# Performance work log

Hardware: AMD Instinct MI355X
Metric: run time of the kernel (lower is better)

Reference implementation:

```python
import jax, jax.numpy as jnp
import numpy as np

B = 65536

def _conv(x, w, stride=(1, 1), padding='VALID', groups=1):
    return jax.lax.conv_general_dilated(
        x, w, window_strides=stride, padding=padding,
        dimension_numbers=('NCHW', 'OIHW', 'NCHW'), feature_group_count=groups)

def _lstm_step(x, h, c, w_ih, w_hh, b_ih, b_hh):
    # PyTorch gate order: i, f, g, o
    gates = x @ w_ih.T + h @ w_hh.T + b_ih + b_hh
    i, f, g, o = jnp.split(gates, 4, axis=-1)
    c_new = jax.nn.sigmoid(f) * c + jax.nn.sigmoid(i) * jnp.tanh(g)
    h_new = jax.nn.sigmoid(o) * jnp.tanh(c_new)
    return h_new, c_new


def setup_inputs() -> dict:
    key = jax.random.key(0)
    ks = jax.random.split(key, 32)
    s = 0.1
    inp = {
        'x': jax.random.normal(ks[0], (B, 3, 41), jnp.float32),
        'lstm1_h': jax.random.normal(ks[1], (B, 64), jnp.float32),
        'lstm1_b': jax.random.normal(ks[2], (B, 64), jnp.float32),
        'lstm2_h': jax.random.normal(ks[3], (B, 64), jnp.float32),
        'lstm2_b': jax.random.normal(ks[4], (B, 64), jnp.float32),
        # conv stack params
        'conv_dw_w': jax.random.normal(ks[5], (1, 1, 3, 3), jnp.float32) * s,
        'conv_pw_w': jax.random.normal(ks[6], (16, 1, 1, 1), jnp.float32) * s,
        'conv_pw_b': jax.random.normal(ks[7], (16,), jnp.float32) * s,
        'sep1_dw_w': jax.random.normal(ks[8], (16, 1, 1, 3), jnp.float32) * s,
        'sep1_pw_w': jax.random.normal(ks[9], (16, 16, 1, 1), jnp.float32) * s,
        'sep1_pw_b': jax.random.normal(ks[10], (16,), jnp.float32) * s,
        'sep2_dw_w': jax.random.normal(ks[11], (16, 1, 1, 3), jnp.float32) * s,
        'sep2_pw_w': jax.random.normal(ks[12], (16, 16, 1, 1), jnp.float32) * s,
        'sep2_pw_b': jax.random.normal(ks[13], (16,), jnp.float32) * s,
        # lstm1: input 80, hidden 64
        'w_ih1': jax.random.normal(ks[14], (256, 80), jnp.float32) * s,
        'w_hh1': jax.random.normal(ks[15], (256, 64), jnp.float32) * s,
        'b_ih1': jax.random.normal(ks[16], (256,), jnp.float32) * s,
        'b_hh1': jax.random.normal(ks[17], (256,), jnp.float32) * s,
        # lstm2: input 64, hidden 64
        'w_ih2': jax.random.normal(ks[18], (256, 64), jnp.float32) * s,
        'w_hh2': jax.random.normal(ks[19], (256, 64), jnp.float32) * s,
        'b_ih2': jax.random.normal(ks[20], (256,), jnp.float32) * s,
        'b_hh2': jax.random.normal(ks[21], (256,), jnp.float32) * s,
        # fc head
        'fc1_w': jax.random.normal(ks[22], (32, 128), jnp.float32) * s,
        'fc1_b': jax.random.normal(ks[23], (32,), jnp.float32) * s,
        'fc2_w': jax.random.normal(ks[24], (1, 32), jnp.float32) * s,
        'fc2_b': jax.random.normal(ks[25], (1,), jnp.float32) * s,
    }
    return inp


def reference(x, lstm1_h, lstm1_b, lstm2_h, lstm2_b,
              conv_dw_w, conv_pw_w, conv_pw_b,
              sep1_dw_w, sep1_pw_w, sep1_pw_b,
              sep2_dw_w, sep2_pw_w, sep2_pw_b,
              w_ih1, w_hh1, b_ih1, b_hh1,
              w_ih2, w_hh2, b_ih2, b_hh2,
              fc1_w, fc1_b, fc2_w, fc2_b):
    b = x.shape[0]
    y = x.reshape(b, 1, 3, 41)
    y = _conv(y, conv_dw_w)                                   # [B,1,1,39]
    y = _conv(y, conv_pw_w) + conv_pw_b[None, :, None, None]  # [B,16,1,39]
    y = jax.nn.relu(y)
    y = jax.lax.reduce_window(y, -jnp.inf, jax.lax.max,
                              (1, 1, 1, 3), (1, 1, 1, 2), 'VALID')  # [B,16,1,19]
    y = _conv(y, sep1_dw_w, stride=(2, 2), padding=((0, 0), (1, 1)), groups=16)  # [B,16,1,10]
    y = _conv(y, sep1_pw_w) + sep1_pw_b[None, :, None, None]
    y = jax.nn.relu(y)
    y = jnp.pad(y, ((0, 0), (0, 0), (0, 0), (0, 1)))          # [B,16,1,11]
    y = _conv(y, sep2_dw_w, stride=(2, 2), groups=16)         # [B,16,1,5]
    y = _conv(y, sep2_pw_w) + sep2_pw_b[None, :, None, None]
    y = jax.nn.relu(y)
    feat = y[:, :, 0, :].transpose(0, 2, 1).reshape(b, 80)    # permute(0,2,1) then flatten W*C
    h1, c1 = _lstm_step(feat, lstm1_h, lstm1_b, w_ih1, w_hh1, b_ih1, b_hh1)
    h2, c2 = _lstm_step(h1, lstm2_h, lstm2_b, w_ih2, w_hh2, b_ih2, b_hh2)
    z = jnp.concatenate([h2, h1], axis=-1)                    # [B,128]
    z = jax.nn.relu(z @ fc1_w.T + fc1_b)
    prob = jax.nn.sigmoid(z @ fc2_w.T + fc2_b)                # [B,1]
    return (prob[:, None, :], h1[None], c1[None], h2[None], c2[None])
```

## Files before the change

kernel.cpp:

```cpp
#include <hip/hip_runtime.h>

typedef unsigned short u16;
typedef __attribute__((ext_vector_type(8))) _Float16 f16x8;
typedef __attribute__((ext_vector_type(4))) float f32x4;

#define NT 256
#define BT 64
#define CBT 32
#define A1S 152
#define H1S 72

__device__ __forceinline__ u16 f2h(float f) {
  _Float16 h = (_Float16)f;
  union { _Float16 h; u16 u; } c; c.h = h; return c.u;
}
__device__ __forceinline__ float sigm(float x) { return 1.0f / (1.0f + __expf(-x)); }
__device__ __forceinline__ float tanh_(float x) {
  float ax = fabsf(x);
  float e = __expf(-2.0f * ax);
  float t = (1.0f - e) / (1.0f + e);
  return copysignf(t, x);
}
__device__ __forceinline__ uint2 packh4(float4 v) {
  return make_uint2((unsigned)f2h(v.x) | ((unsigned)f2h(v.y) << 16),
                    (unsigned)f2h(v.z) | ((unsigned)f2h(v.w) << 16));
}
__device__ __forceinline__ void bar() {
  asm volatile("s_waitcnt lgkmcnt(0)" ::: "memory");
  __builtin_amdgcn_s_barrier();
  asm volatile("" ::: "memory");
}

#define WS_W1   0
#define WS_W2   40960
#define WS_FC1  73728
#define WS_CW   77824
#define WS_BOFF 159744
#define WS_CF   161792
#define WS_FEAT_U16 81088


__global__ __launch_bounds__(NT) void prep(
    const float* __restrict__ wih1, const float* __restrict__ whh1,
    const float* __restrict__ wih2, const float* __restrict__ whh2,
    const float* __restrict__ fc1w,
    const float* __restrict__ bih1, const float* __restrict__ bhh1,
    const float* __restrict__ bih2, const float* __restrict__ bhh2,
    const float* __restrict__ dwWg, const float* __restrict__ pwWg, const float* __restrict__ pwBg,
    const float* __restrict__ s1dwg, const float* __restrict__ s1pwg, const float* __restrict__ s1pbg,
    const float* __restrict__ s2dwg, const float* __restrict__ s2pwg, const float* __restrict__ s2pbg,
    u16* __restrict__ wbf, float* __restrict__ bc, float* __restrict__ cf)
{
  int i = blockIdx.x * NT + threadIdx.x;
  if (i < 40960) {
    int j8 = i & 7, l = (i >> 3) & 63, rem = i >> 9;
    int kc = rem % 5, gw = rem / 5;
    int n = (gw >> 2) * 64 + (gw & 3) * 16 + (l & 15);
    int k = kc * 32 + (l >> 4) * 8 + j8;
    float v = 0.f;
    if (k < 80) v = wih1[n * 80 + k];
    else if (k < 144) v = whh1[n * 64 + (k - 80)];
    wbf[i] = f2h(v);
  } else if (i < 73728) {
    int t2 = i - 40960;
    int j8 = t2 & 7, l = (t2 >> 3) & 63, rem = t2 >> 9;
    int kc = rem & 3, gw = rem >> 2;
    int n = (gw >> 2) * 64 + (gw & 3) * 16 + (l & 15);
    int k = kc * 32 + (l >> 4) * 8 + j8;
    float v = (k < 64) ? wih2[n * 64 + k] : whh2[n * 64 + (k - 64)];
    wbf[i] = f2h(v);
  } else if (i < 77824) {
    int t2 = i - 73728;
    int j8 = t2 & 7, l = (t2 >> 3) & 63, rem = t2 >> 9;
    int kc = rem & 3, nt = rem >> 2;
    int n = nt * 16 + (l & 15);
    int k = kc * 32 + (l >> 4) * 8 + j8;
    int ks = (k < 64) ? k + 64 : k - 64;
    wbf[i] = f2h(fc1w[n * 128 + ks]);
  } else if (i < 79872) {
    int t2 = i - 77824;
    int frag = t2 >> 9, u = t2 & 511;
    int j8 = u & 7, l = (u >> 3) & 63;
    int co = l & 15, kk = (l >> 4) * 8 + j8;
    float v = 0.f;
    if (frag == 0) { int k = kk >> 4, ci = kk & 15; v = s1dwg[ci * 3 + k] * s1pwg[co * 16 + ci]; }
    else if (frag == 1) { if (kk < 16) v = s1dwg[kk * 3 + 2] * s1pwg[co * 16 + kk]; }
    else if (frag == 2) { int k = kk >> 4, ci = kk & 15; v = s2dwg[ci * 3 + k] * s2pwg[co * 16 + ci]; }
    else { if (kk < 16) v = s2dwg[kk * 3 + 2] * s2pwg[co * 16 + kk]; }
    wbf[i] = f2h(v);
  }
  if (i < 256)      bc[i] = bih1[i] + bhh1[i];
  else if (i < 512) bc[i] = bih2[i - 256] + bhh2[i - 256];
  if (i < 89) {
    float v;
    if (i < 16)      { float w = pwWg[i];      v = w > 0.f ? w : 0.f; }
    else if (i < 32) { float w = pwWg[i - 16]; v = w > 0.f ? 0.f : w; }
    else if (i < 48) v = pwBg[i - 32];
    else if (i < 64) v = s1pbg[i - 48];
    else if (i < 80) v = s2pbg[i - 64];
    else             v = dwWg[i - 80];
    cf[i] = v;
  }
}

#define CV_CW   0
#define CV_Y0   384
#define CV_XS   5504
#define CV_P    5504
#define CV_U1   5504
#define CV_FL   384
#define CV_SIZE 27008

__global__ __launch_bounds__(NT, 5) void convk(
    const float* __restrict__ xg, const u16* __restrict__ wbf,
    const float* __restrict__ cf, u16* __restrict__ featg)
{
  __shared__ __align__(16) unsigned char smem[CV_SIZE];
  const int t = threadIdx.x;
  const int blk = blockIdx.x;
  const int base = blk * CBT;

  float* cw = (float*)(smem + CV_CW);
  float* y0 = (float*)(smem + CV_Y0);
  float* xs = (float*)(smem + CV_XS);
  u16* pp  = (u16*)(smem + CV_P);
  u16* u1  = (u16*)(smem + CV_U1);
  u16* fl  = (u16*)(smem + CV_FL);

  const int lane = t & 63, wv = t >> 6, l15 = lane & 15, q16 = lane >> 4;

  const u16* Wf = wbf + WS_CW;
  f16x8 W1a = *(const f16x8*)(Wf + lane * 8);
  f16x8 W1b = *(const f16x8*)(Wf + 512 + lane * 8);
  f16x8 W2a = *(const f16x8*)(Wf + 1024 + lane * 8);
  f16x8 W2b = *(const f16x8*)(Wf + 1536 + lane * 8);

  if (t < 96) cw[t] = (t < 89) ? cf[t] : 0.f;
  {
    const float4* src = (const float4*)xg + (size_t)blk * 984;
    for (int i = t; i < 984; i += NT) *(float4*)(xs + i * 4) = src[i];
  }
  bar();

  {
    float d0 = cw[80], d1 = cw[81], d2 = cw[82], d3 = cw[83], d4 = cw[84],
          d5 = cw[85], d6 = cw[86], d7 = cw[87], d8 = cw[88];
    int b = t >> 3, w0 = (t & 7) * 5;
    const float* xb = xs + b * 123;
    float* yb = y0 + b * 40;
#pragma unroll
    for (int s = 0; s < 5; ++s) {
      int w = w0 + s;
      if (w < 39) {
        float v = d0 * xb[w]      + d1 * xb[w + 1]  + d2 * xb[w + 2]
                + d3 * xb[41 + w] + d4 * xb[42 + w] + d5 * xb[43 + w]
                + d6 * xb[82 + w] + d7 * xb[83 + w] + d8 * xb[84 + w];
        yb[w] = v;
      }
    }
  }
  bar();

  {
    uint4 z; z.x = z.y = z.z = z.w = 0u;
    if (t < 128) {
      int b = t >> 2, sub = t & 3;
      int col = (sub >> 1) ? 20 : 0;
      *(uint4*)(pp + (b * 21 + col) * 16 + (sub & 1) * 8) = z;
    }
    int b = t >> 3, u = t & 7, half = u >> 2, w5b = u & 3;
    float ph[8], pl[8], pb[8];
    ((float4*)ph)[0] = *(float4*)(cw + half * 8);
    ((float4*)ph)[1] = *(float4*)(cw + half * 8 + 4);
    ((float4*)pl)[0] = *(float4*)(cw + 16 + half * 8);
    ((float4*)pl)[1] = *(float4*)(cw + 16 + half * 8 + 4);
    ((float4*)pb)[0] = *(float4*)(cw + 32 + half * 8);
    ((float4*)pb)[1] = *(float4*)(cw + 32 + half * 8 + 4);
    const float* yb = y0 + b * 40;
#pragma unroll
    for (int s = 0; s < 5; ++s) {
      int w5 = w5b + s * 4;
      if (w5 < 19) {
        float a0 = yb[2 * w5], a1 = yb[2 * w5 + 1], a2 = yb[2 * w5 + 2];
        float mx = fmaxf(a0, fmaxf(a1, a2));
        float mn = fminf(a0, fminf(a1, a2));
        unsigned pk[4];
#pragma unroll
        for (int c = 0; c < 4; ++c) {
          float v0 = fmaxf(fmaf(ph[2 * c],     mx, fmaf(pl[2 * c],     mn, pb[2 * c])),     0.f);
          float v1 = fmaxf(fmaf(ph[2 * c + 1], mx, fmaf(pl[2 * c + 1], mn, pb[2 * c + 1])), 0.f);
          pk[c] = (unsigned)f2h(v0) | ((unsigned)f2h(v1) << 16);
        }
        uint4 st; st.x = pk[0]; st.y = pk[1]; st.z = pk[2]; st.w = pk[3];
        *(uint4*)(pp + (b * 21 + w5 + 1) * 16 + half * 8) = st;
      }
    }
  }
  bar();

  f32x4 acc5[5];
  {
    int kA = q16 >> 1, ciA = (q16 & 1) * 8;
#pragma unroll
    for (int s = 0; s < 5; ++s) {
      int tile = wv + s * 4;
      int rowA = tile * 16 + l15;
      int bA = rowA / 10, qA = rowA - bA * 10;
      f16x8 a0 = *(const f16x8*)(pp + (bA * 21 + 2 * qA + kA) * 16 + ciA);
      f16x8 a1 = *(const f16x8*)(pp + (bA * 21 + 2 * qA + 2) * 16 + ciA);
      f32x4 acc = {0.f, 0.f, 0.f, 0.f};
      acc = __builtin_amdgcn_mfma_f32_16x16x32_f16(a0, W1a, acc, 0, 0, 0);
      acc = __builtin_amdgcn_mfma_f32_16x16x32_f16(a1, W1b, acc, 0, 0, 0);
      acc5[s] = acc;
    }
  }
  bar();
  {
    if (t < 64) {
      uint4 z; z.x = z.y = z.z = z.w = 0u;
      *(uint4*)(u1 + ((t >> 1) * 11 + 10) * 16 + (t & 1) * 8) = z;
    }
    float sb1 = cw[48 + l15];
#pragma unroll
    for (int s = 0; s < 5; ++s) {
      int tile = wv + s * 4;
#pragma unroll
      for (int r = 0; r < 4; ++r) {
        int rowg = tile * 16 + q16 * 4 + r;
        int bC = rowg / 10, qC = rowg - bC * 10;
        u1[(bC * 11 + qC) * 16 + l15] = f2h(fmaxf(acc5[s][r] + sb1, 0.f));
      }
    }
  }
  bar();

  {
    float sb2 = cw[64 + l15];
    int kA = q16 >> 1, ciA = (q16 & 1) * 8;
    for (int tile = wv; tile < 10; tile += 4) {
      int rowA = tile * 16 + l15;
      int bA = rowA / 5, rA = rowA - bA * 5;
      f16x8 a0 = *(const f16x8*)(u1 + (bA * 11 + 2 * rA + kA) * 16 + ciA);
      f16x8 a1 = *(const f16x8*)(u1 + (bA * 11 + 2 * rA + 2) * 16 + ciA);
      f32x4 acc = {0.f, 0.f, 0.f, 0.f};
      acc = __builtin_amdgcn_mfma_f32_16x16x32_f16(a0, W2a, acc, 0, 0, 0);
      acc = __builtin_amdgcn_mfma_f32_16x16x32_f16(a1, W2b, acc, 0, 0, 0);
#pragma unroll
      for (int r = 0; r < 4; ++r) {
        int rowg = tile * 16 + q16 * 4 + r;
        int bC = rowg / 5, rC = rowg - bC * 5;
        fl[bC * 80 + rC * 16 + l15] = f2h(fmaxf(acc[r] + sb2, 0.f));
      }
    }
  }
  bar();

  {
    const uint4* s4 = (const uint4*)fl;
    uint4* d4 = (uint4*)(featg + (size_t)base * 80);
    for (int i = t; i < 320; i += NT) d4[i] = s4[i];
  }
}

#define LO_B1   0
#define LO_B2   256
#define LO_FC1B 512
#define LO_FC2W 544
#define LO_FC2B 576
#define LR_A1  2560
#define LR_H1N 22048
#define LSMEM  31264

__global__ __launch_bounds__(NT, 3) void lstmk(
    const float* __restrict__ h1g, const float* __restrict__ c1g,
    const float* __restrict__ h2g, const float* __restrict__ c2g,
    const float* __restrict__ fc1bg, const float* __restrict__ fc2wg, const float* __restrict__ fc2bg,
    const u16* __restrict__ wbf, const float* __restrict__ bc, const u16* __restrict__ featg,
    float* __restrict__ out, int B)
{
  __shared__ __align__(16) unsigned char smem[LSMEM];
  const int t = threadIdx.x;
  const int blk = blockIdx.x;
  const int base = blk * BT;

  float* sw = (float*)smem;
  u16* A1  = (u16*)(smem + LR_A1);
  u16* H1N = (u16*)(smem + LR_H1N);

  float* probO = out;
  float* h1o = out + B;
  float* c1o = out + B + B * 64;
  float* h2o = out + B + B * 128;
  float* c2o = out + B + B * 192;

  const u16* w1f = wbf + WS_W1;
  const u16* w2f = wbf + WS_W2;
  const u16* wFf = wbf + WS_FC1;

  const int w = t >> 6, lane = t & 63, q = lane >> 4, l15 = lane & 15;
  const int j = w * 16 + l15;

  float c1r[16];
#pragma unroll
  for (int mt = 0; mt < 4; ++mt)
#pragma unroll
    for (int r = 0; r < 4; ++r)
      c1r[mt * 4 + r] = c1g[(size_t)(base + mt * 16 + q * 4 + r) * 64 + j];

  uint2 h2p[4];
  {
    const float4* hsrc = (const float4*)h2g + (size_t)blk * 1024;
#pragma unroll
    for (int k = 0; k < 4; ++k) h2p[k] = packh4(hsrc[t + k * 256]);
  }

  for (int i = t; i < 512; i += NT) sw[i] = bc[i];
  for (int i = t; i < 32;  i += NT) sw[LO_FC1B + i] = fc1bg[i];
  for (int i = t; i < 32;  i += NT) sw[LO_FC2W + i] = fc2wg[i];
  if (t == 0) sw[LO_FC2B] = fc2bg[0];
  for (int i = t; i < 640; i += NT) {
    int m = i / 10, o = (i - m * 10) * 8;
    *(uint4*)(A1 + m * A1S + o) = *(const uint4*)(featg + (size_t)(base + m) * 80 + o);
  }
  {
    const float4* hsrc = (const float4*)h1g + (size_t)blk * 1024;
    for (int i = t; i < 1024; i += NT) {
      int m = i >> 4, j4 = (i & 15) * 4;
      *(uint2*)(A1 + m * A1S + 80 + j4) = packh4(hsrc[i]);
    }
  }
  for (int i = t; i < 64; i += NT) {
    uint4 z; z.x = z.y = z.z = z.w = 0u;
    *(uint4*)(A1 + i * A1S + 144) = z;
  }
  if (t == 0) {
    uint4 z; z.x = z.y = z.z = z.w = 0u;
    *(uint4*)(A1 + 64 * A1S) = z;
  }
  bar();

  float c2r[16];

  {
    f16x8 bf1[4][5];
#pragma unroll
    for (int g = 0; g < 4; ++g)
#pragma unroll
      for (int kc = 0; kc < 5; ++kc)
        bf1[g][kc] = *(const f16x8*)(w1f + (size_t)((((g * 4 + w) * 5 + kc) * 64) + lane) * 8);
    float bI = sw[LO_B1 + j], bF = sw[LO_B1 + 64 + j], bG = sw[LO_B1 + 128 + j], bO = sw[LO_B1 + 192 + j];

#pragma unroll 1
    for (int mt = 0; mt < 4; ++mt) {
      f32x4 acc[4];
#pragma unroll
      for (int g = 0; g < 4; ++g) { acc[g][0] = 0.f; acc[g][1] = 0.f; acc[g][2] = 0.f; acc[g][3] = 0.f; }
      const u16* aB = A1 + (mt * 16 + l15) * A1S + q * 8;
#pragma unroll
      for (int kc = 0; kc < 5; ++kc) {
        f16x8 af = *(const f16x8*)(aB + kc * 32);
#pragma unroll
        for (int g = 0; g < 4; ++g)
          acc[g] = __builtin_amdgcn_mfma_f32_16x16x32_f16(af, bf1[g][kc], acc[g], 0, 0, 0);
      }
#pragma unroll
      for (int r = 0; r < 4; ++r) {
        int m = mt * 16 + q * 4 + r;
        int b = base + m;
        float iv = acc[0][r] + bI;
        float fv = acc[1][r] + bF;
        float gv = acc[2][r] + bG;
        float ov = acc[3][r] + bO;
        float cn = sigm(fv) * c1r[mt * 4 + r] + sigm(iv) * tanh_(gv);
        float hn = sigm(ov) * tanh_(cn);
        c1o[b * 64 + j] = cn;
        h1o[b * 64 + j] = hn;
        H1N[m * H1S + j] = f2h(hn);
      }
    }
#pragma unroll
    for (int mt = 0; mt < 4; ++mt)
#pragma unroll
      for (int r = 0; r < 4; ++r)
        c2r[mt * 4 + r] = c2g[(size_t)(base + mt * 16 + q * 4 + r) * 64 + j];
  }
  bar();

  {
#pragma unroll
    for (int k = 0; k < 4; ++k) {
      int i = t + k * 256, m = i >> 4, j4 = (i & 15) * 4;
      *(uint2*)(A1 + m * A1S + 80 + j4) = h2p[k];
    }
  }
  bar();

  {
    f16x8 bf2[4][4];
#pragma unroll
    for (int g = 0; g < 4; ++g)
#pragma unroll
      for (int kc = 0; kc < 4; ++kc)
        bf2[g][kc] = *(const f16x8*)(w2f + (size_t)((((g * 4 + w) * 4 + kc) * 64) + lane) * 8);
    float bI = sw[LO_B2 + j], bF = sw[LO_B2 + 64 + j], bG = sw[LO_B2 + 128 + j], bO = sw[LO_B2 + 192 + j];

#pragma unroll 1
    for (int mt = 0; mt < 4; ++mt) {
      f32x4 acc[4];
#pragma unroll
      for (int g = 0; g < 4; ++g) { acc[g][0] = 0.f; acc[g][1] = 0.f; acc[g][2] = 0.f; acc[g][3] = 0.f; }
      const u16* aB1 = H1N + (mt * 16 + l15) * H1S + q * 8;
      const u16* aB2 = A1 + (mt * 16 + l15) * A1S + 80 + q * 8;
#pragma unroll
      for (int kc = 0; kc < 4; ++kc) {
        f16x8 af = (kc < 2) ? *(const f16x8*)(aB1 + kc * 32)
                            : *(const f16x8*)(aB2 + (kc - 2) * 32);
#pragma unroll
        for (int g = 0; g < 4; ++g)
          acc[g] = __builtin_amdgcn_mfma_f32_16x16x32_f16(af, bf2[g][kc], acc[g], 0, 0, 0);
      }
#pragma unroll
      for (int r = 0; r < 4; ++r) {
        int m = mt * 16 + q * 4 + r;
        int b = base + m;
        float iv = acc[0][r] + bI;
        float fv = acc[1][r] + bF;
        float gv = acc[2][r] + bG;
        float ov = acc[3][r] + bO;
        float cn = sigm(fv) * c2r[mt * 4 + r] + sigm(iv) * tanh_(gv);
        float hn = sigm(ov) * tanh_(cn);
        c2o[b * 64 + j] = cn;
        h2o[b * 64 + j] = hn;
        A1[m * A1S + j] = f2h(hn);
      }
    }
  }
  bar();

  {
    f32x4 accf[2];
#pragma unroll
    for (int nt = 0; nt < 2; ++nt) { accf[nt][0] = 0.f; accf[nt][1] = 0.f; accf[nt][2] = 0.f; accf[nt][3] = 0.f; }
    int m0 = w * 16;
#pragma unroll
    for (int kc = 0; kc < 4; ++kc) {
      f16x8 a = (kc < 2)
        ? *(const f16x8*)(H1N + (m0 + l15) * H1S + kc * 32 + q * 8)
        : *(const f16x8*)(A1 + (m0 + l15) * A1S + (kc - 2) * 32 + q * 8);
#pragma unroll
      for (int nt = 0; nt < 2; ++nt) {
        f16x8 bfr = *(const f16x8*)(wFf + (size_t)(((nt * 4 + kc) * 64) + lane) * 8);
        accf[nt] = __builtin_amdgcn_mfma_f32_16x16x32_f16(a, bfr, accf[nt], 0, 0, 0);
      }
    }
    float fw0 = sw[LO_FC2W + l15], fw1 = sw[LO_FC2W + 16 + l15];
    float fb0 = sw[LO_FC1B + l15], fb1 = sw[LO_FC1B + 16 + l15];
    float f2b = sw[LO_FC2B];
#pragma unroll
    for (int r = 0; r < 4; ++r) {
      float zv0 = fmaxf(accf[0][r] + fb0, 0.f);
      float zv1 = fmaxf(accf[1][r] + fb1, 0.f);
      float part = fmaf(zv0, fw0, zv1 * fw1);
      part += __shfl_xor(part, 1);
      part += __shfl_xor(part, 2);
      part += __shfl_xor(part, 4);
      part += __shfl_xor(part, 8);
      if (l15 == 0) probO[base + m0 + q * 4 + r] = sigm(part + f2b);
    }
  }
}

extern "C" void kernel_launch(void* const* d_in, const int* in_sizes, int n_in,
                              void* d_out, int out_size, void* d_ws, size_t ws_size,
                              hipStream_t stream) {
  (void)n_in; (void)out_size; (void)ws_size;
  int B = in_sizes[0] / 123;
  u16* wbf = (u16*)d_ws;
  float* bcm = (float*)((char*)d_ws + WS_BOFF);
  float* cfm = (float*)((char*)d_ws + WS_CF);
  u16* featg = (u16*)d_ws + WS_FEAT_U16;

  hipLaunchKernelGGL(prep, dim3(312), dim3(NT), 0, stream,
      (const float*)d_in[14], (const float*)d_in[15],
      (const float*)d_in[18], (const float*)d_in[19],
      (const float*)d_in[22],
      (const float*)d_in[16], (const float*)d_in[17],
      (const float*)d_in[20], (const float*)d_in[21],
      (const float*)d_in[5], (const float*)d_in[6], (const float*)d_in[7],
      (const float*)d_in[8], (const float*)d_in[9], (const float*)d_in[10],
      (const float*)d_in[11], (const float*)d_in[12], (const float*)d_in[13],
      wbf, bcm, cfm);

  hipLaunchKernelGGL(convk, dim3(B / CBT), dim3(NT), 0, stream,
      (const float*)d_in[0], wbf, cfm, featg);

  hipLaunchKernelGGL(lstmk, dim3(B / BT), dim3(NT), 0, stream,
      (const float*)d_in[1], (const float*)d_in[2],
      (const float*)d_in[3], (const float*)d_in[4],
      (const float*)d_in[23], (const float*)d_in[24], (const float*)d_in[25],
      wbf, bcm, featg,
      (float*)d_out, B);
}
```

Measured before the change: 247.2 us.

## Fuse conv feature stack and LSTM/FC stages into a single kernel

Merges the conv kernel and the LSTM kernel into one kernel that processes 32 batch rows per block. Conv features are written straight into the shared LSTM input tile instead of going through a global feature buffer, which removes one launch and the global write and read of the features. The trade-off is larger shared memory per block, the same 3-block occupancy bound, half the batch rows per block to amortize weight fragment loads, and half the waves idle in the final FC stage.

Result: slower. 255.2 us (+3.2%).

```diff
diff --git a/kernel.cpp b/kernel.cpp
--- a/kernel.cpp
+++ b/kernel.cpp
@@ -5,8 +5,7 @@
 typedef __attribute__((ext_vector_type(4))) float f32x4;
 
 #define NT 256
-#define BT 64
-#define CBT 32
+#define MBT 32
 #define A1S 152
 #define H1S 72
 
@@ -37,7 +36,6 @@
 #define WS_CW   77824
 #define WS_BOFF 159744
 #define WS_CF   161792
-#define WS_FEAT_U16 81088
 
 
 __global__ __launch_bounds__(NT) void prep(
@@ -103,31 +101,67 @@
   }
 }
 
-#define CV_CW   0
-#define CV_Y0   384
-#define CV_XS   5504
-#define CV_P    5504
-#define CV_U1   5504
-#define CV_FL   384
-#define CV_SIZE 27008
-
-__global__ __launch_bounds__(NT, 5) void convk(
-    const float* __restrict__ xg, const u16* __restrict__ wbf,
-    const float* __restrict__ cf, u16* __restrict__ featg)
+#define LO_B1   0
+#define LO_B2   256
+#define LO_FC1B 512
+#define LO_FC2W 544
+#define LO_FC2B 576
+#define MS_A1   2560
+#define MS_H1N  12320
+#define MS_CW   16928
+#define MS_Y0   17312
+#define MS_XP   22432
+#define MSMEM   43936
+
+__global__ __launch_bounds__(NT, 3) void maink(
+    const float* __restrict__ xg,
+    const float* __restrict__ h1g, const float* __restrict__ c1g,
+    const float* __restrict__ h2g, const float* __restrict__ c2g,
+    const float* __restrict__ fc1bg, const float* __restrict__ fc2wg, const float* __restrict__ fc2bg,
+    const u16* __restrict__ wbf, const float* __restrict__ bc, const float* __restrict__ cf,
+    float* __restrict__ out, int B)
 {
-  __shared__ __align__(16) unsigned char smem[CV_SIZE];
+  __shared__ __align__(16) unsigned char smem[MSMEM];
   const int t = threadIdx.x;
   const int blk = blockIdx.x;
-  const int base = blk * CBT;
-
-  float* cw = (float*)(smem + CV_CW);
-  float* y0 = (float*)(smem + CV_Y0);
-  float* xs = (float*)(smem + CV_XS);
-  u16* pp  = (u16*)(smem + CV_P);
-  u16* u1  = (u16*)(smem + CV_U1);
-  u16* fl  = (u16*)(smem + CV_FL);
-
-  const int lane = t & 63, wv = t >> 6, l15 = lane & 15, q16 = lane >> 4;
+  const int base = blk * MBT;
+
+  float* sw  = (float*)smem;
+  u16* A1  = (u16*)(smem + MS_A1);
+  u16* H1N = (u16*)(smem + MS_H1N);
+  float* cw  = (float*)(smem + MS_CW);
+  float* y0  = (float*)(smem + MS_Y0);
+  float* xs  = (float*)(smem + MS_XP);
+  u16* pp  = (u16*)(smem + MS_XP);
+  u16* u1  = (u16*)(smem + MS_XP);
+
+  float* probO = out;
+  float* h1o = out + B;
+  float* c1o = out + B + B * 64;
+  float* h2o = out + B + B * 128;
+  float* c2o = out + B + B * 192;
+
+  const u16* w1f = wbf + WS_W1;
+  const u16* w2f = wbf + WS_W2;
+  const u16* wFf = wbf + WS_FC1;
+
+  const int wv = t >> 6, lane = t & 63, q = lane >> 4, l15 = lane & 15;
+  const int j = wv * 16 + l15;
+
+  float c1r[8], c2r[8];
+#pragma unroll
+  for (int mt = 0; mt < 2; ++mt)
+#pragma unroll
+    for (int r = 0; r < 4; ++r) {
+      c1r[mt * 4 + r] = c1g[(size_t)(base + mt * 16 + q * 4 + r) * 64 + j];
+      c2r[mt * 4 + r] = c2g[(size_t)(base + mt * 16 + q * 4 + r) * 64 + j];
+    }
+  uint2 h2p[2];
+  {
+    const float4* hsrc = (const float4*)h2g + (size_t)blk * 512;
+#pragma unroll
+    for (int k = 0; k < 2; ++k) h2p[k] = packh4(hsrc[t + k * 256]);
+  }
 
   const u16* Wf = wbf + WS_CW;
   f16x8 W1a = *(const f16x8*)(Wf + lane * 8);
@@ -136,6 +170,25 @@
   f16x8 W2b = *(const f16x8*)(Wf + 1536 + lane * 8);
 
   if (t < 96) cw[t] = (t < 89) ? cf[t] : 0.f;
+  for (int i = t; i < 512; i += NT) sw[i] = bc[i];
+  for (int i = t; i < 32;  i += NT) sw[LO_FC1B + i] = fc1bg[i];
+  for (int i = t; i < 32;  i += NT) sw[LO_FC2W + i] = fc2wg[i];
+  if (t == 0) sw[LO_FC2B] = fc2bg[0];
+  {
+    const float4* hsrc = (const float4*)h1g + (size_t)blk * 512;
+    for (int i = t; i < 512; i += NT) {
+      int m = i >> 4, j4 = (i & 15) * 4;
+      *(uint2*)(A1 + m * A1S + 80 + j4) = packh4(hsrc[i]);
+    }
+  }
+  if (t < 32) {
+    uint4 z; z.x = z.y = z.z = z.w = 0u;
+    *(uint4*)(A1 + t * A1S + 144) = z;
+  }
+  if (t == 32) {
+    uint4 z; z.x = z.y = z.z = z.w = 0u;
+    *(uint4*)(A1 + 32 * A1S) = z;
+  }
   {
     const float4* src = (const float4*)xg + (size_t)blk * 984;
     for (int i = t; i < 984; i += NT) *(float4*)(xs + i * 4) = src[i];
@@ -200,7 +253,7 @@
 
   f32x4 acc5[5];
   {
-    int kA = q16 >> 1, ciA = (q16 & 1) * 8;
+    int kA = q >> 1, ciA = (q & 1) * 8;
 #pragma unroll
     for (int s = 0; s < 5; ++s) {
       int tile = wv + s * 4;
@@ -226,7 +279,7 @@
       int tile = wv + s * 4;
 #pragma unroll
       for (int r = 0; r < 4; ++r) {
-        int rowg = tile * 16 + q16 * 4 + r;
+        int rowg = tile * 16 + q * 4 + r;
         int bC = rowg / 10, qC = rowg - bC * 10;
         u1[(bC * 11 + qC) * 16 + l15] = f2h(fmaxf(acc5[s][r] + sb1, 0.f));
       }
@@ -236,7 +289,7 @@
 
   {
     float sb2 = cw[64 + l15];
-    int kA = q16 >> 1, ciA = (q16 & 1) * 8;
+    int kA = q >> 1, ciA = (q & 1) * 8;
     for (int tile = wv; tile < 10; tile += 4) {
       int rowA = tile * 16 + l15;
       int bA = rowA / 5, rA = rowA - bA * 5;
@@ -247,99 +300,13 @@
       acc = __builtin_amdgcn_mfma_f32_16x16x32_f16(a1, W2b, acc, 0, 0, 0);
 #pragma unroll
       for (int r = 0; r < 4; ++r) {
-        int rowg = tile * 16 + q16 * 4 + r;
+        int rowg = tile * 16 + q * 4 + r;
         int bC = rowg / 5, rC = rowg - bC * 5;
-        fl[bC * 80 + rC * 16 + l15] = f2h(fmaxf(acc[r] + sb2, 0.f));
-      }
-    }
-  }
-  bar();
-
-  {
-    const uint4* s4 = (const uint4*)fl;
-    uint4* d4 = (uint4*)(featg + (size_t)base * 80);
-    for (int i = t; i < 320; i += NT) d4[i] = s4[i];
-  }
-}
-
-#define LO_B1   0
-#define LO_B2   256
-#define LO_FC1B 512
-#define LO_FC2W 544
-#define LO_FC2B 576
-#define LR_A1  2560
-#define LR_H1N 22048
-#define LSMEM  31264
-
-__global__ __launch_bounds__(NT, 3) void lstmk(
-    const float* __restrict__ h1g, const float* __restrict__ c1g,
-    const float* __restrict__ h2g, const float* __restrict__ c2g,
-    const float* __restrict__ fc1bg, const float* __restrict__ fc2wg, const float* __restrict__ fc2bg,
-    const u16* __restrict__ wbf, const float* __restrict__ bc, const u16* __restrict__ featg,
-    float* __restrict__ out, int B)
-{
-  __shared__ __align__(16) unsigned char smem[LSMEM];
-  const int t = threadIdx.x;
-  const int blk = blockIdx.x;
-  const int base = blk * BT;
-
-  float* sw = (float*)smem;
-  u16* A1  = (u16*)(smem + LR_A1);
-  u16* H1N = (u16*)(smem + LR_H1N);
-
-  float* probO = out;
-  float* h1o = out + B;
-  float* c1o = out + B + B * 64;
-  float* h2o = out + B + B * 128;
-  float* c2o = out + B + B * 192;
-
-  const u16* w1f = wbf + WS_W1;
-  const u16* w2f = wbf + WS_W2;
-  const u16* wFf = wbf + WS_FC1;
-
-  const int w = t >> 6, lane = t & 63, q = lane >> 4, l15 = lane & 15;
-  const int j = w * 16 + l15;
-
-  float c1r[16];
-#pragma unroll
-  for (int mt = 0; mt < 4; ++mt)
-#pragma unroll
-    for (int r = 0; r < 4; ++r)
-      c1r[mt * 4 + r] = c1g[(size_t)(base + mt * 16 + q * 4 + r) * 64 + j];
-
-  uint2 h2p[4];
-  {
-    const float4* hsrc = (const float4*)h2g + (size_t)blk * 1024;
-#pragma unroll
-    for (int k = 0; k < 4; ++k) h2p[k] = packh4(hsrc[t + k * 256]);
-  }
-
-  for (int i = t; i < 512; i += NT) sw[i] = bc[i];
-  for (int i = t; i < 32;  i += NT) sw[LO_FC1B + i] = fc1bg[i];
-  for (int i = t; i < 32;  i += NT) sw[LO_FC2W + i] = fc2wg[i];
-  if (t == 0) sw[LO_FC2B] = fc2bg[0];
-  for (int i = t; i < 640; i += NT) {
-    int m = i / 10, o = (i - m * 10) * 8;
-    *(uint4*)(A1 + m * A1S + o) = *(const uint4*)(featg + (size_t)(base + m) * 80 + o);
-  }
-  {
-    const float4* hsrc = (const float4*)h1g + (size_t)blk * 1024;
-    for (int i = t; i < 1024; i += NT) {
-      int m = i >> 4, j4 = (i & 15) * 4;
-      *(uint2*)(A1 + m * A1S + 80 + j4) = packh4(hsrc[i]);
-    }
-  }
-  for (int i = t; i < 64; i += NT) {
-    uint4 z; z.x = z.y = z.z = z.w = 0u;
-    *(uint4*)(A1 + i * A1S + 144) = z;
-  }
-  if (t == 0) {
-    uint4 z; z.x = z.y = z.z = z.w = 0u;
-    *(uint4*)(A1 + 64 * A1S) = z;
-  }
-  bar();
-
-  float c2r[16];
+        A1[bC * A1S + rC * 16 + l15] = f2h(fmaxf(acc[r] + sb2, 0.f));
+      }
+    }
+  }
+  bar();
 
   {
     f16x8 bf1[4][5];
@@ -347,11 +314,11 @@
     for (int g = 0; g < 4; ++g)
 #pragma unroll
       for (int kc = 0; kc < 5; ++kc)
-        bf1[g][kc] = *(const f16x8*)(w1f + (size_t)((((g * 4 + w) * 5 + kc) * 64) + lane) * 8);
+        bf1[g][kc] = *(const f16x8*)(w1f + (size_t)((((g * 4 + wv) * 5 + kc) * 64) + lane) * 8);
     float bI = sw[LO_B1 + j], bF = sw[LO_B1 + 64 + j], bG = sw[LO_B1 + 128 + j], bO = sw[LO_B1 + 192 + j];
 
 #pragma unroll 1
-    for (int mt = 0; mt < 4; ++mt) {
+    for (int mt = 0; mt < 2; ++mt) {
       f32x4 acc[4];
 #pragma unroll
       for (int g = 0; g < 4; ++g) { acc[g][0] = 0.f; acc[g][1] = 0.f; acc[g][2] = 0.f; acc[g][3] = 0.f; }
@@ -378,17 +345,12 @@
         H1N[m * H1S + j] = f2h(hn);
       }
     }
-#pragma unroll
-    for (int mt = 0; mt < 4; ++mt)
-#pragma unroll
-      for (int r = 0; r < 4; ++r)
-        c2r[mt * 4 + r] = c2g[(size_t)(base + mt * 16 + q * 4 + r) * 64 + j];
-  }
-  bar();
-
-  {
-#pragma unroll
-    for (int k = 0; k < 4; ++k) {
+  }
+  bar();
+
+  {
+#pragma unroll
+    for (int k = 0; k < 2; ++k) {
       int i = t + k * 256, m = i >> 4, j4 = (i & 15) * 4;
       *(uint2*)(A1 + m * A1S + 80 + j4) = h2p[k];
     }
@@ -401,11 +363,11 @@
     for (int g = 0; g < 4; ++g)
 #pragma unroll
       for (int kc = 0; kc < 4; ++kc)
-        bf2[g][kc] = *(const f16x8*)(w2f + (size_t)((((g * 4 + w) * 4 + kc) * 64) + lane) * 8);
+        bf2[g][kc] = *(const f16x8*)(w2f + (size_t)((((g * 4 + wv) * 4 + kc) * 64) + lane) * 8);
     float bI = sw[LO_B2 + j], bF = sw[LO_B2 + 64 + j], bG = sw[LO_B2 + 128 + j], bO = sw[LO_B2 + 192 + j];
 
 #pragma unroll 1
-    for (int mt = 0; mt < 4; ++mt) {
+    for (int mt = 0; mt < 2; ++mt) {
       f32x4 acc[4];
 #pragma unroll
       for (int g = 0; g < 4; ++g) { acc[g][0] = 0.f; acc[g][1] = 0.f; acc[g][2] = 0.f; acc[g][3] = 0.f; }
@@ -437,11 +399,11 @@
   }
   bar();
 
-  {
+  if (wv < 2) {
     f32x4 accf[2];
 #pragma unroll
     for (int nt = 0; nt < 2; ++nt) { accf[nt][0] = 0.f; accf[nt][1] = 0.f; accf[nt][2] = 0.f; accf[nt][3] = 0.f; }
-    int m0 = w * 16;
+    int m0 = wv * 16;
 #pragma unroll
     for (int kc = 0; kc < 4; ++kc) {
       f16x8 a = (kc < 2)
@@ -478,7 +440,6 @@
   u16* wbf = (u16*)d_ws;
   float* bcm = (float*)((char*)d_ws + WS_BOFF);
   float* cfm = (float*)((char*)d_ws + WS_CF);
-  u16* featg = (u16*)d_ws + WS_FEAT_U16;
 
   hipLaunchKernelGGL(prep, dim3(312), dim3(NT), 0, stream,
       (const float*)d_in[14], (const float*)d_in[15],
@@ -491,13 +452,11 @@
       (const float*)d_in[11], (const float*)d_in[12], (const float*)d_in[13],
       wbf, bcm, cfm);
 
-  hipLaunchKernelGGL(convk, dim3(B / CBT), dim3(NT), 0, stream,
-      (const float*)d_in[0], wbf, cfm, featg);
-
-  hipLaunchKernelGGL(lstmk, dim3(B / BT), dim3(NT), 0, stream,
+  hipLaunchKernelGGL(maink, dim3(B / MBT), dim3(NT), 0, stream,
+      (const float*)d_in[0],
       (const float*)d_in[1], (const float*)d_in[2],
       (const float*)d_in[3], (const float*)d_in[4],
       (const float*)d_in[23], (const float*)d_in[24], (const float*)d_in[25],
-      wbf, bcm, featg,
+      wbf, bcm, cfm,
       (float*)d_out, B);
 }
```

## Stage LSTM cell and hidden states in LDS for coalesced float4 I/O

Applied to the files above, without the earlier changes.

Loads c1/c2 with coalesced float4 reads into fp16 LDS tiles instead of strided per-thread scalar loads. The h1/c1/h2/c2 outputs are staged in LDS and written back as coalesced float4 stores after the second LSTM, replacing scattered scalar global stores. This trades extra LDS use (lower occupancy headroom) for better global memory coalescing. The old cell state and all four outputs are now rounded through fp16, which reduces precision of the returned c1, c2, h1 and h2.

Result: faster. 231.0 us (-6.6%).

```diff
diff --git a/kernel.cpp b/kernel.cpp
--- a/kernel.cpp
+++ b/kernel.cpp
@@ -9,10 +9,14 @@
 #define CBT 32
 #define A1S 152
 #define H1S 72
+#define CFS 68
 
 __device__ __forceinline__ u16 f2h(float f) {
   _Float16 h = (_Float16)f;
   union { _Float16 h; u16 u; } c; c.h = h; return c.u;
+}
+__device__ __forceinline__ float h2f(u16 v) {
+  union { u16 u; _Float16 h; } c; c.u = v; return (float)c.h;
 }
 __device__ __forceinline__ float sigm(float x) { return 1.0f / (1.0f + __expf(-x)); }
 __device__ __forceinline__ float tanh_(float x) {
@@ -24,6 +28,12 @@
 __device__ __forceinline__ uint2 packh4(float4 v) {
   return make_uint2((unsigned)f2h(v.x) | ((unsigned)f2h(v.y) << 16),
                     (unsigned)f2h(v.z) | ((unsigned)f2h(v.w) << 16));
+}
+__device__ __forceinline__ float4 unph4(uint2 p) {
+  float4 r;
+  r.x = h2f((u16)(p.x & 0xffff)); r.y = h2f((u16)(p.x >> 16));
+  r.z = h2f((u16)(p.y & 0xffff)); r.w = h2f((u16)(p.y >> 16));
+  return r;
 }
 __device__ __forceinline__ void bar() {
   asm volatile("s_waitcnt lgkmcnt(0)" ::: "memory");
@@ -267,9 +277,11 @@
 #define LO_FC1B 512
 #define LO_FC2W 544
 #define LO_FC2B 576
-#define LR_A1  2560
-#define LR_H1N 22048
-#define LSMEM  31264
+#define LR_A1   2560
+#define LR_H1N  22048
+#define LR_C1F  31264
+#define LR_C2F  39968
+#define LSMEM   48672
 
 __global__ __launch_bounds__(NT, 3) void lstmk(
     const float* __restrict__ h1g, const float* __restrict__ c1g,
@@ -286,6 +298,8 @@
   float* sw = (float*)smem;
   u16* A1  = (u16*)(smem + LR_A1);
   u16* H1N = (u16*)(smem + LR_H1N);
+  u16* c1f = (u16*)(smem + LR_C1F);
+  u16* c2f = (u16*)(smem + LR_C2F);
 
   float* probO = out;
   float* h1o = out + B;
@@ -300,20 +314,22 @@
   const int w = t >> 6, lane = t & 63, q = lane >> 4, l15 = lane & 15;
   const int j = w * 16 + l15;
 
-  float c1r[16];
-#pragma unroll
-  for (int mt = 0; mt < 4; ++mt)
-#pragma unroll
-    for (int r = 0; r < 4; ++r)
-      c1r[mt * 4 + r] = c1g[(size_t)(base + mt * 16 + q * 4 + r) * 64 + j];
-
+  {
+    const float4* c1src = (const float4*)c1g + (size_t)blk * 1024;
+    const float4* c2src = (const float4*)c2g + (size_t)blk * 1024;
+#pragma unroll
+    for (int k = 0; k < 4; ++k) {
+      int i = t + k * 256, row = i >> 4, c4 = (i & 15) * 4;
+      *(uint2*)(c1f + row * CFS + c4) = packh4(c1src[i]);
+      *(uint2*)(c2f + row * CFS + c4) = packh4(c2src[i]);
+    }
+  }
   uint2 h2p[4];
   {
     const float4* hsrc = (const float4*)h2g + (size_t)blk * 1024;
 #pragma unroll
     for (int k = 0; k < 4; ++k) h2p[k] = packh4(hsrc[t + k * 256]);
   }
-
   for (int i = t; i < 512; i += NT) sw[i] = bc[i];
   for (int i = t; i < 32;  i += NT) sw[LO_FC1B + i] = fc1bg[i];
   for (int i = t; i < 32;  i += NT) sw[LO_FC2W + i] = fc2wg[i];
@@ -339,8 +355,6 @@
   }
   bar();
 
-  float c2r[16];
-
   {
     f16x8 bf1[4][5];
 #pragma unroll
@@ -366,23 +380,17 @@
 #pragma unroll
       for (int r = 0; r < 4; ++r) {
         int m = mt * 16 + q * 4 + r;
-        int b = base + m;
         float iv = acc[0][r] + bI;
         float fv = acc[1][r] + bF;
         float gv = acc[2][r] + bG;
         float ov = acc[3][r] + bO;
-        float cn = sigm(fv) * c1r[mt * 4 + r] + sigm(iv) * tanh_(gv);
+        float cold = h2f(c1f[m * CFS + j]);
+        float cn = sigm(fv) * cold + sigm(iv) * tanh_(gv);
         float hn = sigm(ov) * tanh_(cn);
-        c1o[b * 64 + j] = cn;
-        h1o[b * 64 + j] = hn;
+        c1f[m * CFS + j] = f2h(cn);
         H1N[m * H1S + j] = f2h(hn);
       }
     }
-#pragma unroll
-    for (int mt = 0; mt < 4; ++mt)
-#pragma unroll
-      for (int r = 0; r < 4; ++r)
-        c2r[mt * 4 + r] = c2g[(size_t)(base + mt * 16 + q * 4 + r) * 64 + j];
   }
   bar();
 
@@ -422,20 +430,31 @@
 #pragma unroll
       for (int r = 0; r < 4; ++r) {
         int m = mt * 16 + q * 4 + r;
-        int b = base + m;
         float iv = acc[0][r] + bI;
         float fv = acc[1][r] + bF;
         float gv = acc[2][r] + bG;
         float ov = acc[3][r] + bO;
-        float cn = sigm(fv) * c2r[mt * 4 + r] + sigm(iv) * tanh_(gv);
+        float cold = h2f(c2f[m * CFS + j]);
+        float cn = sigm(fv) * cold + sigm(iv) * tanh_(gv);
         float hn = sigm(ov) * tanh_(cn);
-        c2o[b * 64 + j] = cn;
-        h2o[b * 64 + j] = hn;
+        c2f[m * CFS + j] = f2h(cn);
         A1[m * A1S + j] = f2h(hn);
       }
     }
   }
   bar();
+
+  {
+#pragma unroll
+    for (int k = 0; k < 4; ++k) {
+      int i = t + k * 256, row = i >> 4, c4 = (i & 15) * 4;
+      size_t gb = (size_t)(base + row) * 64 + c4;
+      *(float4*)(h1o + gb) = unph4(*(const uint2*)(H1N + row * H1S + c4));
+      *(float4*)(c1o + gb) = unph4(*(const uint2*)(c1f + row * CFS + c4));
+      *(float4*)(h2o + gb) = unph4(*(const uint2*)(A1 + row * A1S + c4));
+      *(float4*)(c2o + gb) = unph4(*(const uint2*)(c2f + row * CFS + c4));
+    }
+  }
 
   {
     f32x4 accf[2];
```
